# Optimization experiments

Hardware: AMD Instinct MI355X
Metric: run time of the kernel (lower is better)

The kernel has to match this reference:

```python
import jax, jax.numpy as jnp
import numpy as np
from jax import lax

EPS = 0.1  # regularization_strength, 'kl' regularization (torchsort.soft_rank)


@jax.jit
def _pav_kl(s, logw):
    """Batched pool-adjacent-violators for KL-regularized isotonic regression.
    s: [B, n] (rows sorted descending), logw: [n] = log([n, n-1, ..., 1]).
    Port of torchsort's isotonic_kl kernel; the sequential algorithm is
    flattened so each while-loop iteration performs one step per row.
    Returns (sol [B,n] block-constant dual solution, block_id [B,n])."""
    B, n = s.shape
    rows = jnp.arange(B)
    w = jnp.broadcast_to(logw, (B, n))

    def g(A, idx):  # batched gather with clipped index
        return A[rows, jnp.clip(idx, 0, n - 1)]

    def cond(st):
        return jnp.any(st[0] < n)

    def body(st):
        i, k, sol_prev, merging, target, lse_y, lse_w, sol = st
        active = i < n
        scan_mode = active & ~merging
        k_nm = g(target, i) + 1
        at_end = k_nm >= n
        decreasing = g(sol, i) > g(sol, k_nm)
        advance = scan_mode & (at_end | decreasing)
        start_merge = scan_mode & ~at_end & ~decreasing

        # one merge step for rows currently merging: pool block at i with block at k
        ly = jnp.logaddexp(g(lse_y, i), g(lse_y, k))
        lw = jnp.logaddexp(g(lse_w, i), g(lse_w, k))
        k_next = g(target, k) + 1
        stop = merging & ((k_next >= n) | (sol_prev > g(sol, k_next)))

        wi = jnp.where(merging, i, 0)  # inactive rows write back old value
        lse_y = lse_y.at[rows, wi].set(jnp.where(merging, ly, lse_y[rows, wi]))
        lse_w = lse_w.at[rows, wi].set(jnp.where(merging, lw, lse_w[rows, wi]))
        sol = sol.at[rows, wi].set(jnp.where(merging, ly - lw, sol[rows, wi]))

        p1 = jnp.where(stop, i, 0)
        target = target.at[rows, p1].set(jnp.where(stop, k_next - 1, target[rows, p1]))
        p2 = jnp.where(stop, jnp.clip(k_next - 1, 0, n - 1), 0)
        target = target.at[rows, p2].set(jnp.where(stop, i, target[rows, p2]))

        i_back = jnp.where(i > 0, g(target, i - 1), i)  # pool with preceding block
        i_new = jnp.where(advance, k_nm, jnp.where(stop, i_back, i))
        k_new = jnp.where(start_merge, k_nm, jnp.where(merging & ~stop, k_next, k))
        merging_new = (merging & ~stop) | start_merge
        sol_prev_new = jnp.where(start_merge, g(sol, i), sol_prev)
        return (i_new, k_new, sol_prev_new, merging_new, target, lse_y, lse_w, sol)

    init = (jnp.zeros(B, jnp.int32), jnp.zeros(B, jnp.int32),
            jnp.zeros(B, s.dtype), jnp.zeros(B, bool),
            jnp.broadcast_to(jnp.arange(n, dtype=jnp.int32), (B, n)).copy(),
            s, w, s - w)
    _, _, _, _, target, _, _, sol = lax.while_loop(cond, body, init)

    # reconstruct block-constant solution and per-position block ids
    def recon(carry, xs):
        block_end, val, bid = carry
        j, sol_j, tgt_j = xs
        newb = j > block_end
        val = jnp.where(newb, sol_j, val)
        block_end = jnp.where(newb, tgt_j, block_end)
        bid = bid + newb.astype(jnp.int32)
        return (block_end, val, bid), (val, bid)

    carry0 = (jnp.full(B, -1, jnp.int32), sol[:, 0], jnp.full(B, -1, jnp.int32))
    _, (sol_full, block_id) = lax.scan(
        recon, carry0, (jnp.arange(n, dtype=jnp.int32), sol.T, target.T))
    return sol_full.T, block_id.T


def _soft_rank_core(x):
    # x: [B, n] -> soft ranks [B, n]  (torchsort.soft_rank, 'kl')
    B, n = x.shape
    theta = x / EPS
    perm = jnp.argsort(-theta, axis=-1)  # stable descending sort
    s = jnp.take_along_axis(theta, perm, axis=-1)
    logw = jnp.log(jnp.arange(n, 0, -1).astype(x.dtype))  # log([n..1])
    sol, block_id = _pav_kl(s, logw)
    r_sorted = jnp.exp(s - sol)  # = softmax(s_block) * sum(w_block)
    inv = jnp.argsort(perm, axis=-1)
    ranks = jnp.take_along_axis(r_sorted, inv, axis=-1)
    return ranks, (r_sorted, inv, perm, block_id)


def soft_rank_kl(x):
    return _soft_rank_core(x)[0]


def setup_inputs() -> dict:
    key = jax.random.key(0)
    k1, k2 = jax.random.split(key)
    x1 = jax.random.normal(k1, (16, 256, 2048), dtype=jnp.float32)
    x2 = jax.random.normal(k2, (16, 256, 2048), dtype=jnp.float32)
    return {"x1": x1, "x2": x2}


def reference(x1, x2):
    S, T, V = x1.shape  # n_sents, trg_length, scored dim
    r1 = soft_rank_kl(x1.reshape(-1, V))
    r2 = soft_rank_kl(x2.reshape(-1, V))
    c1 = r1 - jnp.mean(r1, axis=-1, keepdims=True)
    c2 = r2 - jnp.mean(r2, axis=-1, keepdims=True)
    corr = jnp.sum(c1 * c2, axis=-1) / (
        jnp.linalg.norm(c1, axis=-1) * jnp.linalg.norm(c2, axis=-1))
    return (1.0 - corr).reshape(S, T)
```

## Files before the change

kernel.cpp:

```cpp
#include <hip/hip_runtime.h>
#include <math.h>

#define N   2048
#define NT  256
#define V   8

__device__ __forceinline__ int wsum(int h, int e) {
    return (((N - h) + (N - e)) * (e - h + 1)) >> 1;
}

__device__ __forceinline__ int pidx(int j) { return j + (j >> 5); }

__device__ __forceinline__ unsigned desc_key(float t) {
    unsigned u = __float_as_uint(t);
    unsigned a = (u & 0x80000000u) ? ~u : (u ^ 0x80000000u);
    return ~a;
}
__device__ __forceinline__ float decode_key(unsigned d) {
    unsigned a = ~d;
    unsigned u = (a & 0x80000000u) ? (a ^ 0x80000000u) : ~a;
    return __uint_as_float(u);
}

#define INVALID_P 0xFFFFFFFFu
__device__ __forceinline__ unsigned packYH(float Y, int h) {
    return ((__float_as_uint(Y) + 0x400u) & 0xFFFFF800u) | (unsigned)h;
}
__device__ __forceinline__ float upY(unsigned u) { return __uint_as_float(u & 0xFFFFF800u); }
__device__ __forceinline__ int   upH(unsigned u) { return (int)(u & 0x7FFu); }

__device__ __forceinline__ void ceu(unsigned &a, unsigned &b, bool up) {
    unsigned mn = (a < b) ? a : b;
    unsigned mx = (a < b) ? b : a;
    a = up ? mn : mx;
    b = up ? mx : mn;
}

__device__ __forceinline__ void merge8(unsigned* r, bool up) {
    ceu(r[0], r[4], up); ceu(r[1], r[5], up); ceu(r[2], r[6], up); ceu(r[3], r[7], up);
    ceu(r[0], r[2], up); ceu(r[1], r[3], up); ceu(r[4], r[6], up); ceu(r[5], r[7], up);
    ceu(r[0], r[1], up); ceu(r[2], r[3], up); ceu(r[4], r[5], up); ceu(r[6], r[7], up);
}

__device__ __forceinline__ void shfl_ce(unsigned* r, int d, bool keepMin) {
    #pragma unroll
    for (int q = 0; q < V; ++q) {
        unsigned p = __shfl_xor(r[q], d, 64);
        bool lt = r[q] < p;
        r[q] = (lt == keepMin) ? r[q] : p;
    }
}

__device__ __forceinline__ int next_head_p(const unsigned* sU,
                                           const unsigned char* sBeg,
                                           const unsigned char* sEnd,
                                           int lane, int d, int bEnd)
{
    if (d + 1 < (int)sEnd[lane]) return upH(sU[(d + 1) * NT + lane]);
    for (int l = lane + 1; l < bEnd; ++l)
        if (sBeg[l] != sEnd[l]) return upH(sU[(int)sBeg[l] * NT + l]);
    return bEnd << 3;
}

__global__ void __launch_bounds__(NT, 8)
fused_kernel(const float* __restrict__ x1, const float* __restrict__ x2,
             float* __restrict__ out)
{
    __shared__ unsigned      s_kx[N + (N >> 5)];
    __shared__ unsigned      s_u [N + (N >> 5)];
    __shared__ unsigned char sBeg[NT], sEnd[NT];
    __shared__ float         s_red[NT / 64][5];
    __shared__ unsigned      swF[NT / 64];
    __shared__ int           swB[NT / 64];

    float* s_rf = (float*)s_u;

    const int p    = blockIdx.x;
    const int tid  = threadIdx.x;
    const int lane = tid & 63;
    const int wid  = tid >> 6;

    float S1 = 0.f, Q1 = 0.f, S2 = 0.f, Q2 = 0.f, P = 0.f;
    float rv1[V];

    for (int ph = 0; ph < 2; ++ph) {
        const float* __restrict__ x = ph ? x2 : x1;
        const size_t base = (size_t)p * N;

        const float4* __restrict__ xv = (const float4*)(x + base + tid * V);
        float4 a0 = xv[0], a1 = xv[1];
        unsigned r[V];
        r[0] = desc_key(a0.x * 10.0f); r[1] = desc_key(a0.y * 10.0f);
        r[2] = desc_key(a0.z * 10.0f); r[3] = desc_key(a0.w * 10.0f);
        r[4] = desc_key(a1.x * 10.0f); r[5] = desc_key(a1.y * 10.0f);
        r[6] = desc_key(a1.z * 10.0f); r[7] = desc_key(a1.w * 10.0f);

        ceu(r[0], r[1], true);  ceu(r[2], r[3], false);
        ceu(r[4], r[5], true);  ceu(r[6], r[7], false);
        ceu(r[0], r[2], true);  ceu(r[1], r[3], true);
        ceu(r[4], r[6], false); ceu(r[5], r[7], false);
        ceu(r[0], r[1], true);  ceu(r[2], r[3], true);
        ceu(r[4], r[5], false); ceu(r[6], r[7], false);
        merge8(r, (tid & 1) == 0);

        #pragma unroll
        for (int kk = 4; kk <= 11; ++kk) {
            const int k  = 1 << kk;
            const bool up = ((tid & (k >> 3)) == 0);
            #pragma unroll
            for (int jb = kk - 1; jb >= 3; --jb) {
                const int jj = 1 << jb;
                const int d  = jj >> 3;
                if (d >= 64) {
                    __syncthreads();
                    #pragma unroll
                    for (int q = 0; q < V; ++q) s_kx[pidx(tid * V + q)] = r[q];
                    __syncthreads();
                    const bool keepMin = (up == ((tid & d) == 0));
                    const int ptid = tid ^ d;
                    #pragma unroll
                    for (int q = 0; q < V; ++q) {
                        unsigned pv = s_kx[pidx(ptid * V + q)];
                        bool lt = r[q] < pv;
                        r[q] = (lt == keepMin) ? r[q] : pv;
                    }
                } else {
                    shfl_ce(r, d, up == ((tid & d) == 0));
                }
            }
            merge8(r, up);
        }

        __syncthreads();
        #pragma unroll
        for (int q = 0; q < V; ++q) s_kx[pidx(tid * V + q)] = r[q];

        {
            int   sp = 0;
            float t0Y = 0.f, t1Y = 0.f;
            int   t0h = 0,   t1h = 0;
            const int bse = tid * V;
            #pragma unroll
            for (int k = 0; k < V; ++k) {
                const int j = bse + k;
                float cY = __expf(decode_key(s_kx[pidx(j)]));
                int   ch = j;
                while (sp > 0) {
                    float cW = (float)wsum(ch, j);
                    float tW = (float)wsum(t0h, ch - 1);
                    if (t0Y * cW > cY * tW) break;
                    cY += t0Y; ch = t0h;
                    --sp;
                    t0Y = t1Y; t0h = t1h;
                    if (sp > 1) {
                        unsigned u = s_u[(sp - 2) * NT + tid];
                        t1Y = upY(u); t1h = upH(u);
                    }
                }
                s_u[sp * NT + tid] = packYH(cY, ch);
                t1Y = t0Y; t1h = t0h;
                t0Y = cY;  t0h = ch;
                ++sp;
            }
            sBeg[tid] = 0; sEnd[tid] = (unsigned char)sp;
        }
        __syncthreads();

        for (int lev = 0; lev < 8; ++lev) {
            const int g = 1 << lev;
            if ((tid & (2 * g - 1)) == 0) {
                const int a = tid, mid = tid + g, b = tid + 2 * g;
                int l0 = mid - 1;
                while (l0 >= a && sBeg[l0] == sEnd[l0]) --l0;
                int l1 = mid;
                while (l1 < b && sBeg[l1] == sEnd[l1]) ++l1;
                if (l0 >= a && l1 < b) {
                    int d0 = (int)sEnd[l0] - 1;
                    unsigned tu = s_u[d0 * NT + l0];
                    float tY = upY(tu); int th_ = upH(tu);
                    int te = (mid << 3) - 1;
                    int d1 = (int)sBeg[l1];
                    unsigned cu = s_u[d1 * NT + l1];
                    float cY = upY(cu); int ch = upH(cu);
                    int ce = next_head_p(s_u, sBeg, sEnd, l1, d1, b) - 1;
                    if (!(tY * (float)wsum(ch, ce) > cY * (float)wsum(th_, te))) {
                        sBeg[l1] = (unsigned char)(d1 + 1);
                        for (;;) {
                            if (l0 >= a &&
                                !(tY * (float)wsum(ch, ce) > cY * (float)wsum(th_, te))) {
                                cY += tY; ch = th_;
                                sEnd[l0] = (unsigned char)((int)sEnd[l0] - 1);
                                if (sBeg[l0] == sEnd[l0]) {
                                    do { --l0; } while (l0 >= a && sBeg[l0] == sEnd[l0]);
                                }
                                if (l0 >= a) {
                                    int dd = (int)sEnd[l0] - 1;
                                    unsigned uu = s_u[dd * NT + l0];
                                    tY = upY(uu); te = th_ - 1; th_ = upH(uu);
                                }
                                continue;
                            }
                            while (l1 < b && sBeg[l1] == sEnd[l1]) ++l1;
                            if (l1 < b) {
                                int dn = (int)sBeg[l1];
                                unsigned nu = s_u[dn * NT + l1];
                                float nY = upY(nu); int nh = upH(nu);
                                int ne = next_head_p(s_u, sBeg, sEnd, l1, dn, b) - 1;
                                if (!(cY * (float)wsum(nh, ne) > nY * (float)wsum(ch, ce))) {
                                    cY += nY; ce = ne;
                                    sBeg[l1] = (unsigned char)(dn + 1);
                                    continue;
                                }
                            }
                            break;
                        }
                        int lh = ch >> 3;
                        if (ch >= (mid << 3)) {
                            int nb = (int)sBeg[lh] - 1;
                            sBeg[lh] = (unsigned char)nb;
                            s_u[nb * NT + lh] = packYH(cY, ch);
                        } else {
                            int nb2 = (int)sEnd[lh];
                            s_u[nb2 * NT + lh] = packYH(cY, ch);
                            sEnd[lh] = (unsigned char)(nb2 + 1);
                        }
                    }
                }
            }
            __syncthreads();
        }

        const int b0 = sBeg[tid], b1 = sEnd[tid];
        unsigned stReg[V];
        #pragma unroll
        for (int d = 0; d < V; ++d) stReg[d] = s_u[d * NT + tid];
        unsigned myLast  = (b1 > b0) ? stReg[b1 - 1] : INVALID_P;
        int      myFirst = (b1 > b0) ? upH(stReg[b0]) : N;

        unsigned fv = myLast;
        #pragma unroll
        for (int off = 1; off < 64; off <<= 1) {
            unsigned o = (unsigned)__shfl_up((int)fv, off);
            if (fv == INVALID_P) fv = o;
        }
        unsigned cF = (unsigned)__shfl_up((int)fv, 1);
        if (lane == 0) cF = INVALID_P;
        int bv = myFirst;
        #pragma unroll
        for (int off = 1; off < 64; off <<= 1) {
            int o = __shfl_down(bv, off);
            if (bv == N) bv = o;
        }
        int cB = __shfl_down(bv, 1);
        if (lane == 63) cB = N;
        if (lane == 63) swF[wid] = fv;
        if (lane == 0)  swB[wid] = bv;
        __syncthreads();
        if (cF == INVALID_P)
            for (int w = wid - 1; w >= 0; --w)
                if (swF[w] != INVALID_P) { cF = swF[w]; break; }
        if (cB == N)
            for (int w = wid + 1; w < NT / 64; ++w)
                if (swB[w] != N) { cB = swB[w]; break; }

        {
            int dptr = b0;
            int nxtOwn = (dptr < b1) ? upH(stReg[dptr]) : N;
            unsigned cur = cF;
            #pragma unroll
            for (int q = 0; q < V; ++q) {
                int j = tid * V + q;
                if (j == nxtOwn) {
                    cur = stReg[dptr];
                    ++dptr;
                    nxtOwn = (dptr < b1) ? upH(stReg[dptr]) : N;
                }
                s_u[pidx(j)] = cur;
            }
        }
        {
            int dptr2 = b1 - 1;
            int nxt = cB;
            #pragma unroll
            for (int q = V - 1; q >= 0; --q) {
                int j = tid * V + q;
                int e = nxt - 1;
                unsigned cu = s_u[pidx(j)];
                float c  = (float)wsum(upH(cu), e) / upY(cu);
                float rv = __expf(decode_key(s_kx[pidx(j)])) * c;
                s_rf[pidx(j)] = rv;
                if (dptr2 >= b0 && upH(stReg[dptr2]) == j) { nxt = j; --dptr2; }
            }
        }
        __syncthreads();

        {
            float4 c0 = xv[0], c1 = xv[1];
            float xx[V] = {c0.x, c0.y, c0.z, c0.w, c1.x, c1.y, c1.z, c1.w};
            #pragma unroll
            for (int q = 0; q < V; ++q) {
                unsigned dv = desc_key(xx[q] * 10.0f);
                int lo = 0, hi = N - 1;
                #pragma unroll
                for (int it = 0; it < 11; ++it) {
                    int mid = (lo + hi) >> 1;
                    if (s_kx[pidx(mid)] < dv) lo = mid + 1; else hi = mid;
                }
                float rv = s_rf[pidx(lo)];
                if (ph == 0) {
                    rv1[q] = rv;
                    S1 += rv; Q1 += rv * rv;
                } else {
                    S2 += rv; Q2 += rv * rv; P += rv1[q] * rv;
                }
            }
        }
        __syncthreads();
    }

    #pragma unroll
    for (int off = 32; off > 0; off >>= 1) {
        S1 += __shfl_down(S1, off);
        Q1 += __shfl_down(Q1, off);
        S2 += __shfl_down(S2, off);
        Q2 += __shfl_down(Q2, off);
        P  += __shfl_down(P,  off);
    }
    if (lane == 0) {
        s_red[wid][0] = S1; s_red[wid][1] = Q1; s_red[wid][2] = S2;
        s_red[wid][3] = Q2; s_red[wid][4] = P;
    }
    __syncthreads();
    if (tid == 0) {
        for (int w = 1; w < NT / 64; ++w) {
            S1 += s_red[w][0]; Q1 += s_red[w][1]; S2 += s_red[w][2];
            Q2 += s_red[w][3]; P  += s_red[w][4];
        }
        const float inv_n = 1.0f / (float)N;
        float num = P  - S1 * S2 * inv_n;
        float d1  = Q1 - S1 * S1 * inv_n;
        float d2  = Q2 - S2 * S2 * inv_n;
        out[p] = 1.0f - num / sqrtf(d1 * d2);
    }
}

extern "C" void kernel_launch(void* const* d_in, const int* in_sizes, int n_in,
                              void* d_out, int out_size, void* d_ws, size_t ws_size,
                              hipStream_t stream) {
    const float* x1 = (const float*)d_in[0];
    const float* x2 = (const float*)d_in[1];
    float* out = (float*)d_out;
    const int nrows = in_sizes[0] / N;
    fused_kernel<<<nrows, NT, 0, stream>>>(x1, x2, out);
}
```

Before: 300.7 us.

## Carry original index in sort keys to replace binary-search rank lookup with scatter

Sort keys now embed each element's original index in their low 11 bits, so the bitonic sort directly yields the permutation. Full-precision keys are stored in shared memory by original position and gathered via the embedded index. Final rank values are scattered back to original positions, eliminating the per-element 11-step binary search over shared memory. This trades quantized sort keys (coarser ordering of near-ties) and additional barriers for removing the inverse-permutation search.

New measurement: 287.1 us. 1.05x faster.

```diff
diff --git a/kernel.cpp b/kernel.cpp
--- a/kernel.cpp
+++ b/kernel.cpp
@@ -20,6 +20,10 @@
     unsigned a = ~d;
     unsigned u = (a & 0x80000000u) ? (a ^ 0x80000000u) : ~a;
     return __uint_as_float(u);
+}
+
+__device__ __forceinline__ unsigned qkey(float t, int j) {
+    return ((desc_key(t) + 0x400u) & 0xFFFFF800u) | (unsigned)j;
 }
 
 #define INVALID_P 0xFFFFFFFFu
@@ -73,7 +77,7 @@
     __shared__ unsigned      swF[NT / 64];
     __shared__ int           swB[NT / 64];
 
-    float* s_rf = (float*)s_u;
+    float* s_kxf = (float*)s_kx;
 
     const int p    = blockIdx.x;
     const int tid  = threadIdx.x;
@@ -89,11 +93,12 @@
 
         const float4* __restrict__ xv = (const float4*)(x + base + tid * V);
         float4 a0 = xv[0], a1 = xv[1];
+        const int bse = tid * V;
         unsigned r[V];
-        r[0] = desc_key(a0.x * 10.0f); r[1] = desc_key(a0.y * 10.0f);
-        r[2] = desc_key(a0.z * 10.0f); r[3] = desc_key(a0.w * 10.0f);
-        r[4] = desc_key(a1.x * 10.0f); r[5] = desc_key(a1.y * 10.0f);
-        r[6] = desc_key(a1.z * 10.0f); r[7] = desc_key(a1.w * 10.0f);
+        r[0] = qkey(a0.x * 10.0f, bse + 0); r[1] = qkey(a0.y * 10.0f, bse + 1);
+        r[2] = qkey(a0.z * 10.0f, bse + 2); r[3] = qkey(a0.w * 10.0f, bse + 3);
+        r[4] = qkey(a1.x * 10.0f, bse + 4); r[5] = qkey(a1.y * 10.0f, bse + 5);
+        r[6] = qkey(a1.z * 10.0f, bse + 6); r[7] = qkey(a1.w * 10.0f, bse + 7);
 
         ceu(r[0], r[1], true);  ceu(r[2], r[3], false);
         ceu(r[4], r[5], true);  ceu(r[6], r[7], false);
@@ -132,18 +137,36 @@
         }
 
         __syncthreads();
-        #pragma unroll
-        for (int q = 0; q < V; ++q) s_kx[pidx(tid * V + q)] = r[q];
-
-        {
+
+        {
+            float4 c0 = xv[0], c1 = xv[1];
+            s_kx[pidx(bse + 0)] = desc_key(c0.x * 10.0f);
+            s_kx[pidx(bse + 1)] = desc_key(c0.y * 10.0f);
+            s_kx[pidx(bse + 2)] = desc_key(c0.z * 10.0f);
+            s_kx[pidx(bse + 3)] = desc_key(c0.w * 10.0f);
+            s_kx[pidx(bse + 4)] = desc_key(c1.x * 10.0f);
+            s_kx[pidx(bse + 5)] = desc_key(c1.y * 10.0f);
+            s_kx[pidx(bse + 6)] = desc_key(c1.z * 10.0f);
+            s_kx[pidx(bse + 7)] = desc_key(c1.w * 10.0f);
+        }
+        __syncthreads();
+
+        {
+            unsigned fkv[V];
+            #pragma unroll
+            for (int k = 0; k < V; ++k)
+                fkv[k] = s_kx[pidx((int)(r[k] & 0x7FFu))];
+            float eY[V];
+            #pragma unroll
+            for (int k = 0; k < V; ++k) eY[k] = __expf(decode_key(fkv[k]));
+
             int   sp = 0;
             float t0Y = 0.f, t1Y = 0.f;
             int   t0h = 0,   t1h = 0;
-            const int bse = tid * V;
             #pragma unroll
             for (int k = 0; k < V; ++k) {
                 const int j = bse + k;
-                float cY = __expf(decode_key(s_kx[pidx(j)]));
+                float cY = eY[k];
                 int   ch = j;
                 while (sp > 0) {
                     float cW = (float)wsum(ch, j);
@@ -278,7 +301,14 @@
                 s_u[pidx(j)] = cur;
             }
         }
-        {
+
+        {
+            unsigned fkv2[V];
+            #pragma unroll
+            for (int q = 0; q < V; ++q)
+                fkv2[q] = s_kx[pidx((int)(r[q] & 0x7FFu))];
+            __syncthreads();
+
             int dptr2 = b1 - 1;
             int nxt = cB;
             #pragma unroll
@@ -287,26 +317,17 @@
                 int e = nxt - 1;
                 unsigned cu = s_u[pidx(j)];
                 float c  = (float)wsum(upH(cu), e) / upY(cu);
-                float rv = __expf(decode_key(s_kx[pidx(j)])) * c;
-                s_rf[pidx(j)] = rv;
+                float rv = __expf(decode_key(fkv2[q])) * c;
+                s_kxf[pidx((int)(r[q] & 0x7FFu))] = rv;
                 if (dptr2 >= b0 && upH(stReg[dptr2]) == j) { nxt = j; --dptr2; }
             }
         }
         __syncthreads();
 
         {
-            float4 c0 = xv[0], c1 = xv[1];
-            float xx[V] = {c0.x, c0.y, c0.z, c0.w, c1.x, c1.y, c1.z, c1.w};
             #pragma unroll
             for (int q = 0; q < V; ++q) {
-                unsigned dv = desc_key(xx[q] * 10.0f);
-                int lo = 0, hi = N - 1;
-                #pragma unroll
-                for (int it = 0; it < 11; ++it) {
-                    int mid = (lo + hi) >> 1;
-                    if (s_kx[pidx(mid)] < dv) lo = mid + 1; else hi = mid;
-                }
-                float rv = s_rf[pidx(lo)];
+                float rv = s_kxf[pidx(bse + q)];
                 if (ph == 0) {
                     rv1[q] = rv;
                     S1 += rv; Q1 += rv * rv;
```
